# Performance work log

Measured on AMD Instinct MI355X. Metric: run time of the kernel, lower is better.

The kernel has to match this reference:

```python
import jax, jax.numpy as jnp
import numpy as np

HIDDEN = 20


def setup_inputs() -> dict:
    key = jax.random.key(0)
    ks = jax.random.split(key, 8)
    B, T = 8192, 2048
    x = jax.random.normal(ks[0], (B, T), dtype=jnp.float32)
    # linear1: 1 -> HIDDEN
    W1 = jax.random.normal(ks[1], (HIDDEN, 1), dtype=jnp.float32) * 0.5
    b1 = jax.random.normal(ks[2], (HIDDEN,), dtype=jnp.float32) * 0.1
    # LSTMCell(HIDDEN, HIDDEN): torch layout [4*H, H], gate order i,f,g,o
    W_ih = jax.random.normal(ks[3], (4 * HIDDEN, HIDDEN), dtype=jnp.float32) * 0.2
    W_hh = jax.random.normal(ks[4], (4 * HIDDEN, HIDDEN), dtype=jnp.float32) * 0.2
    b_ih = jax.random.normal(ks[5], (4 * HIDDEN,), dtype=jnp.float32) * 0.1
    b_hh = jax.random.normal(ks[6], (4 * HIDDEN,), dtype=jnp.float32) * 0.1
    # linear2: HIDDEN -> 1
    W2 = jax.random.normal(ks[7], (1, HIDDEN), dtype=jnp.float32) * 0.2
    b2 = jnp.zeros((1,), dtype=jnp.float32)
    return {"input": x, "W1": W1, "b1": b1, "W_ih": W_ih, "W_hh": W_hh,
            "b_ih": b_ih, "b_hh": b_hh, "W2": W2, "b2": b2}


def reference(input, W1, b1, W_ih, W_hh, b_ih, b_hh, W2, b2):
    B, T = input.shape
    h0 = jnp.zeros((B, HIDDEN), dtype=input.dtype)
    c0 = jnp.zeros((B, HIDDEN), dtype=input.dtype)

    def step(carry, x_t):
        h, c = carry
        # linear1 on scalar input: [B] -> [B, HIDDEN]
        hid = x_t[:, None] * W1[:, 0][None, :] + b1
        # LSTMCell gates, torch order: i, f, g, o
        gates = hid @ W_ih.T + b_ih + h @ W_hh.T + b_hh  # [B, 4H]
        i_g, f_g, g_g, o_g = jnp.split(gates, 4, axis=-1)
        c_new = jax.nn.sigmoid(f_g) * c + jax.nn.sigmoid(i_g) * jnp.tanh(g_g)
        h_new = jax.nn.sigmoid(o_g) * jnp.tanh(c_new)
        out = h_new @ W2.T + b2  # [B, 1]
        return (h_new, c_new), out[:, 0]

    xs = input.T  # [T, B]
    _, outs = jax.lax.scan(step, (h0, c0), xs)  # outs: [T, B]
    return outs.T  # [B, T]
```

## Files before the change

### kernel.cpp

```cpp
#include <hip/hip_runtime.h>


#define HID 20
#define ROWS_PER_WAVE 3
#define NTHREADS 64
#define L2E 1.4426950408889634f

typedef float v2f __attribute__((ext_vector_type(2)));

__device__ __forceinline__ float exp2_hw(float v) { return __builtin_amdgcn_exp2f(v); }
__device__ __forceinline__ float rcp_hw(float v)  { return __builtin_amdgcn_rcpf(v); }

__device__ __forceinline__ float sig_s(float gs) {
    return rcp_hw(1.0f + exp2_hw(-gs));
}
__device__ __forceinline__ float tanh_2Ls(float gs2) {
    return (2.0f * L2E) - (4.0f * L2E) * rcp_hw(1.0f + exp2_hw(gs2));
}
__device__ __forceinline__ float tanh_c(float cs) {
    return 1.0f - 2.0f * rcp_hw(1.0f + exp2_hw(cs));
}

__global__ __attribute__((amdgpu_flat_work_group_size(NTHREADS, NTHREADS),
                          amdgpu_waves_per_eu(3, 3)))
void lstm_wave(
        const float* __restrict__ x,
        const float* __restrict__ W1,
        const float* __restrict__ b1,
        const float* __restrict__ W_ih,
        const float* __restrict__ W_hh,
        const float* __restrict__ b_ih,
        const float* __restrict__ b_hh,
        const float* __restrict__ W2,
        const float* __restrict__ b2,
        float* __restrict__ out,
        const int B, const int T)
{
    const int lane = threadIdx.x;
    const int lrow = lane / HID;
    const int m    = lane % HID;
    const bool outlane = (lrow == 3) && (m < ROWS_PER_WAVE);
    const int rslot = (lrow == 3) ? m : lrow;
    const long rowbase = (long)blockIdx.x * ROWS_PER_WAVE;
    const long row = rowbase + ((lrow == 3) ? (long)((m < 3) ? m : 0) : (long)lrow);
    const long arow = (row < B) ? row : (B - 1);
    const bool ovalid = outlane && (row < B);

    __shared__ __align__(16) float hbuf[2][ROWS_PER_WAVE + 1][HID];

    float u[4], v[4];
    if (lrow < 3) {
#pragma unroll
        for (int g = 0; g < 4; ++g) {
            const int j = g * HID + m;
            const float s = (g == 2) ? (2.0f * L2E) : L2E;
            float uu = 0.f, vv = 0.f;
#pragma unroll
            for (int k = 0; k < HID; ++k) {
                const float wi = W_ih[j * HID + k];
                uu += wi * W1[k];
                vv += wi * b1[k];
            }
            u[g] = s * uu;
            v[g] = s * (vv + b_ih[j] + b_hh[j]);
        }
    } else {
#pragma unroll
        for (int g = 0; g < 4; ++g) { u[g] = 0.f; v[g] = 0.f; }
        v[0] = b2[0];
    }

    v2f whh2[4][HID / 2];
    if (lrow < 3) {
#pragma unroll
        for (int g = 0; g < 4; ++g) {
            const int j = g * HID + m;
            const float s = (g == 2) ? (2.0f * L2E) : L2E;
#pragma unroll
            for (int kk = 0; kk < HID / 2; ++kk) {
                v2f w;
                w.x = s * W_hh[j * HID + 2 * kk];
                w.y = s * W_hh[j * HID + 2 * kk + 1];
                whh2[g][kk] = w;
            }
        }
    } else {
#pragma unroll
        for (int kk = 0; kk < HID / 2; ++kk) {
            v2f w; w.x = W2[2 * kk]; w.y = W2[2 * kk + 1];
            whh2[0][kk] = w;
            whh2[1][kk] = (v2f)(0.f);
            whh2[2][kk] = (v2f)(0.f);
            whh2[3][kk] = (v2f)(0.f);
        }
    }

#pragma unroll
    for (int g = 0; g < 4; ++g)
#pragma unroll
        for (int kk = 0; kk < HID / 2; ++kk)
            asm volatile("" : "+v"(whh2[g][kk]));

    float cs = 0.f;
    hbuf[0][lrow][m] = 0.f;
    hbuf[1][lrow][m] = 0.f;
    __syncthreads();

    const float* __restrict__ xrow = x   + arow * T;
    float* __restrict__       orow = out + arow * T;

    const float4* __restrict__ rd0 = (const float4*)&hbuf[0][rslot][0];
    const float4* __restrict__ rd1 = (const float4*)&hbuf[1][rslot][0];
    float* __restrict__ wr0 = &hbuf[1][lrow][m];
    float* __restrict__ wr1 = &hbuf[0][lrow][m];

    float xv_next = xrow[0];

#define GATE_BODY(RD, WR, OUT_IDX_VALID, OUT_IDX)                               \
    {                                                                            \
        v2f a0, a1, a2, a3;                                                      \
        a0.x = v[0] + xv * u[0]; a0.y = 0.f;                                     \
        a1.x = v[1] + xv * u[1]; a1.y = 0.f;                                     \
        a2.x = v[2] + xv * u[2]; a2.y = 0.f;                                     \
        a3.x = v[3] + xv * u[3]; a3.y = 0.f;                                     \
        _Pragma("unroll")                                                        \
        for (int q = 0; q < 5; ++q) {                                            \
            const float4 f = RD[q];                                              \
            v2f hA; hA.x = f.x; hA.y = f.y;                                      \
            v2f hB; hB.x = f.z; hB.y = f.w;                                      \
            a0 = __builtin_elementwise_fma(whh2[0][2*q],   hA, a0);              \
            a1 = __builtin_elementwise_fma(whh2[1][2*q],   hA, a1);              \
            a2 = __builtin_elementwise_fma(whh2[2][2*q],   hA, a2);              \
            a3 = __builtin_elementwise_fma(whh2[3][2*q],   hA, a3);              \
            a0 = __builtin_elementwise_fma(whh2[0][2*q+1], hB, a0);              \
            a1 = __builtin_elementwise_fma(whh2[1][2*q+1], hB, a1);              \
            a2 = __builtin_elementwise_fma(whh2[2][2*q+1], hB, a2);              \
            a3 = __builtin_elementwise_fma(whh2[3][2*q+1], hB, a3);              \
        }                                                                        \
        const float g0 = a0.x + a0.y;                                            \
        const float g1 = a1.x + a1.y;                                            \
        const float g2 = a2.x + a2.y;                                            \
        const float g3 = a3.x + a3.y;                                            \
        if ((OUT_IDX_VALID) && ovalid) orow[OUT_IDX] = g0;                       \
        const float ig  = sig_s(g0);                                             \
        const float fg  = sig_s(g1);                                             \
        const float ggs = tanh_2Ls(g2);                                          \
        const float og  = sig_s(g3);                                             \
        cs = fg * cs + ig * ggs;                                                 \
        *(WR) = og * tanh_c(cs);                                                 \
        __syncthreads();                                                         \
    }

    for (int t = 0; t < T; t += 2) {
        {
            const float xv = xv_next;
            xv_next = xrow[t + 1];
            GATE_BODY(rd0, wr0, t > 0, t - 1)
        }
        {
            const float xv = xv_next;
            const int tn = (t + 2 < T) ? (t + 2) : (T - 1);
            xv_next = xrow[tn];
            GATE_BODY(rd1, wr1, true, t)
        }
    }

    if (ovalid) {
        float o = v[0];
#pragma unroll
        for (int q = 0; q < 5; ++q) {
            const float4 f = rd0[q];
            o += whh2[0][2*q].x   * f.x + whh2[0][2*q].y   * f.y
               + whh2[0][2*q+1].x * f.z + whh2[0][2*q+1].y * f.w;
        }
        orow[T - 1] = o;
    }
#undef GATE_BODY
}

extern "C" void kernel_launch(void* const* d_in, const int* in_sizes, int n_in,
                              void* d_out, int out_size, void* d_ws, size_t ws_size,
                              hipStream_t stream) {
    (void)n_in; (void)d_ws; (void)ws_size; (void)out_size;
    const float* x    = (const float*)d_in[0];
    const float* W1   = (const float*)d_in[1];
    const float* b1   = (const float*)d_in[2];
    const float* W_ih = (const float*)d_in[3];
    const float* W_hh = (const float*)d_in[4];
    const float* b_ih = (const float*)d_in[5];
    const float* b_hh = (const float*)d_in[6];
    const float* W2   = (const float*)d_in[7];
    const float* b2   = (const float*)d_in[8];
    float* out        = (float*)d_out;

    const int B = 8192;
    const int T = in_sizes[0] / B;
    const int grid = (B + ROWS_PER_WAVE - 1) / ROWS_PER_WAVE;

    lstm_wave<<<grid, NTHREADS, 0, stream>>>(x, W1, b1, W_ih, W_hh, b_ih, b_hh, W2, b2, out, B, T);
}
```

Measured before the change: 1.191 ms.

## Drop per-step barriers with single LDS buffer and batch x/out in float4

```diff
diff --git a/kernel.cpp b/kernel.cpp
--- a/kernel.cpp
+++ b/kernel.cpp
@@ -46,7 +46,7 @@
     const long arow = (row < B) ? row : (B - 1);
     const bool ovalid = outlane && (row < B);
 
-    __shared__ __align__(16) float hbuf[2][ROWS_PER_WAVE + 1][HID];
+    __shared__ __align__(16) float hbuf[ROWS_PER_WAVE + 1][HID];
 
     float u[4], v[4];
     if (lrow < 3) {
@@ -102,80 +102,86 @@
             asm volatile("" : "+v"(whh2[g][kk]));
 
     float cs = 0.f;
-    hbuf[0][lrow][m] = 0.f;
-    hbuf[1][lrow][m] = 0.f;
-    __syncthreads();
+    hbuf[lrow][m] = 0.f;
+    if (lane < HID) hbuf[3][lane] = 0.f;
 
     const float* __restrict__ xrow = x   + arow * T;
     float* __restrict__       orow = out + arow * T;
 
-    const float4* __restrict__ rd0 = (const float4*)&hbuf[0][rslot][0];
-    const float4* __restrict__ rd1 = (const float4*)&hbuf[1][rslot][0];
-    float* __restrict__ wr0 = &hbuf[1][lrow][m];
-    float* __restrict__ wr1 = &hbuf[0][lrow][m];
-
-    float xv_next = xrow[0];
-
-#define GATE_BODY(RD, WR, OUT_IDX_VALID, OUT_IDX)                               \
-    {                                                                            \
-        v2f a0, a1, a2, a3;                                                      \
-        a0.x = v[0] + xv * u[0]; a0.y = 0.f;                                     \
-        a1.x = v[1] + xv * u[1]; a1.y = 0.f;                                     \
-        a2.x = v[2] + xv * u[2]; a2.y = 0.f;                                     \
-        a3.x = v[3] + xv * u[3]; a3.y = 0.f;                                     \
-        _Pragma("unroll")                                                        \
-        for (int q = 0; q < 5; ++q) {                                            \
-            const float4 f = RD[q];                                              \
-            v2f hA; hA.x = f.x; hA.y = f.y;                                      \
-            v2f hB; hB.x = f.z; hB.y = f.w;                                      \
-            a0 = __builtin_elementwise_fma(whh2[0][2*q],   hA, a0);              \
-            a1 = __builtin_elementwise_fma(whh2[1][2*q],   hA, a1);              \
-            a2 = __builtin_elementwise_fma(whh2[2][2*q],   hA, a2);              \
-            a3 = __builtin_elementwise_fma(whh2[3][2*q],   hA, a3);              \
-            a0 = __builtin_elementwise_fma(whh2[0][2*q+1], hB, a0);              \
-            a1 = __builtin_elementwise_fma(whh2[1][2*q+1], hB, a1);              \
-            a2 = __builtin_elementwise_fma(whh2[2][2*q+1], hB, a2);              \
-            a3 = __builtin_elementwise_fma(whh2[3][2*q+1], hB, a3);              \
-        }                                                                        \
-        const float g0 = a0.x + a0.y;                                            \
-        const float g1 = a1.x + a1.y;                                            \
-        const float g2 = a2.x + a2.y;                                            \
-        const float g3 = a3.x + a3.y;                                            \
-        if ((OUT_IDX_VALID) && ovalid) orow[OUT_IDX] = g0;                       \
-        const float ig  = sig_s(g0);                                             \
-        const float fg  = sig_s(g1);                                             \
-        const float ggs = tanh_2Ls(g2);                                          \
-        const float og  = sig_s(g3);                                             \
-        cs = fg * cs + ig * ggs;                                                 \
-        *(WR) = og * tanh_c(cs);                                                 \
-        __syncthreads();                                                         \
-    }
-
-    for (int t = 0; t < T; t += 2) {
-        {
-            const float xv = xv_next;
-            xv_next = xrow[t + 1];
-            GATE_BODY(rd0, wr0, t > 0, t - 1)
-        }
-        {
-            const float xv = xv_next;
-            const int tn = (t + 2 < T) ? (t + 2) : (T - 1);
-            xv_next = xrow[tn];
-            GATE_BODY(rd1, wr1, true, t)
-        }
-    }
-
-    if (ovalid) {
+    const float4* __restrict__ rdp = (const float4*)&hbuf[rslot][0];
+    float* __restrict__        wrp = &hbuf[lrow][m];
+
+    float4 F0 = rdp[0], F1 = rdp[1], F2 = rdp[2], F3 = rdp[3], F4 = rdp[4];
+
+    float4 xq = *(const float4*)&xrow[0];
+    float4 xq_next;
+    float4 obuf = make_float4(0.f, 0.f, 0.f, 0.f);
+
+#define FQ(Q, FF)                                                               \
+    {   v2f hA; hA.x = (FF).x; hA.y = (FF).y;                                   \
+        v2f hB; hB.x = (FF).z; hB.y = (FF).w;                                   \
+        a0 = __builtin_elementwise_fma(whh2[0][2*Q],   hA, a0);                 \
+        a1 = __builtin_elementwise_fma(whh2[1][2*Q],   hA, a1);                 \
+        a2 = __builtin_elementwise_fma(whh2[2][2*Q],   hA, a2);                 \
+        a3 = __builtin_elementwise_fma(whh2[3][2*Q],   hA, a3);                 \
+        a0 = __builtin_elementwise_fma(whh2[0][2*Q+1], hB, a0);                 \
+        a1 = __builtin_elementwise_fma(whh2[1][2*Q+1], hB, a1);                 \
+        a2 = __builtin_elementwise_fma(whh2[2][2*Q+1], hB, a2);                 \
+        a3 = __builtin_elementwise_fma(whh2[3][2*Q+1], hB, a3);                 }
+
+#define BODY(XV, OSLOT)                                                         \
+    {                                                                           \
+        const float xv = (XV);                                                  \
+        v2f a0, a1, a2, a3;                                                     \
+        a0.x = v[0] + xv * u[0]; a0.y = 0.f;                                    \
+        a1.x = v[1] + xv * u[1]; a1.y = 0.f;                                    \
+        a2.x = v[2] + xv * u[2]; a2.y = 0.f;                                    \
+        a3.x = v[3] + xv * u[3]; a3.y = 0.f;                                    \
+        FQ(0, F0) FQ(1, F1) FQ(2, F2) FQ(3, F3) FQ(4, F4)                       \
+        const float g0 = a0.x + a0.y;                                           \
+        const float g1 = a1.x + a1.y;                                           \
+        const float g2 = a2.x + a2.y;                                           \
+        const float g3 = a3.x + a3.y;                                           \
+        OSLOT = g0;                                                             \
+        const float ig  = sig_s(g0);                                            \
+        const float fg  = sig_s(g1);                                            \
+        const float ggs = tanh_2Ls(g2);                                         \
+        const float og  = sig_s(g3);                                            \
+        cs = fg * cs + ig * ggs;                                                \
+        *wrp = og * tanh_c(cs);                                                 \
+        F0 = rdp[0]; F1 = rdp[1]; F2 = rdp[2]; F3 = rdp[3]; F4 = rdp[4];        \
+    }
+
+    for (int t = 0; t < T; t += 4) {
+        const int tp = (t + 4 < T) ? (t + 4) : t;
+        xq_next = *(const float4*)&xrow[tp];
+
+        BODY(xq.x, obuf.w)
+        if (t >= 4 && ovalid) *(float4*)&orow[t - 4] = obuf;
+        BODY(xq.y, obuf.x)
+        BODY(xq.z, obuf.y)
+        BODY(xq.w, obuf.z)
+
+        xq = xq_next;
+    }
+
+    {
         float o = v[0];
-#pragma unroll
-        for (int q = 0; q < 5; ++q) {
-            const float4 f = rd0[q];
-            o += whh2[0][2*q].x   * f.x + whh2[0][2*q].y   * f.y
-               + whh2[0][2*q+1].x * f.z + whh2[0][2*q+1].y * f.w;
-        }
-        orow[T - 1] = o;
-    }
-#undef GATE_BODY
+        o += whh2[0][0].x * F0.x + whh2[0][0].y * F0.y
+           + whh2[0][1].x * F0.z + whh2[0][1].y * F0.w;
+        o += whh2[0][2].x * F1.x + whh2[0][2].y * F1.y
+           + whh2[0][3].x * F1.z + whh2[0][3].y * F1.w;
+        o += whh2[0][4].x * F2.x + whh2[0][4].y * F2.y
+           + whh2[0][5].x * F2.z + whh2[0][5].y * F2.w;
+        o += whh2[0][6].x * F3.x + whh2[0][6].y * F3.y
+           + whh2[0][7].x * F3.z + whh2[0][7].y * F3.w;
+        o += whh2[0][8].x * F4.x + whh2[0][8].y * F4.y
+           + whh2[0][9].x * F4.z + whh2[0][9].y * F4.w;
+        obuf.w = o;
+        if (ovalid) *(float4*)&orow[T - 4] = obuf;
+    }
+#undef BODY
+#undef FQ
 }
 
 extern "C" void kernel_launch(void* const* d_in, const int* in_sizes, int n_in,
```

Result: faster. 1.077 ms (-9.6%).
